# Kernel optimization log

Hardware: AMD Instinct MI355X
Metric: run time of the kernel (lower is better)

Reference implementation:

```python
import jax, jax.numpy as jnp
import numpy as np

EPS = 1e-5

def bn_lastdim(x, g, b):
    # BatchNorm2d (training-mode batch stats) applied over all axes except last channel axis
    m = x.mean(axis=(0, 1, 2), keepdims=True)
    v = x.var(axis=(0, 1, 2), keepdims=True)
    return g * (x - m) * jax.lax.rsqrt(v + EPS) + b

def setup_inputs() -> dict:
    key = jax.random.key(0)
    ks = jax.random.split(key, 8)
    B, N, M, F1, K = 8, 8192, 2048, 64, 32
    PF, OUT, DIV = 64, 128, 4
    IN_CH = PF + F1  # 128
    inp = {
        "points": jax.random.normal(ks[0], (B, N, 3), jnp.float32),
        "queries": jax.random.normal(ks[1], (B, M, 3), jnp.float32),
        "feat_prev": jax.random.normal(ks[2], (B, N, F1), jnp.float32),
        # Lift params: linear1 3->32, linear2 32->64
        "w1": jax.random.normal(ks[3], (3, PF // 2), jnp.float32) * 0.1,
        "b1": jnp.zeros((PF // 2,), jnp.float32),
        "w2": jax.random.normal(ks[4], (PF // 2, PF), jnp.float32) * 0.1,
        "b2": jnp.zeros((PF,), jnp.float32),
        # batchnorm affine params (bn1 over 3, bn2 over 32, bn3 over in_channel)
        "g1": jnp.ones((3,), jnp.float32), "be1": jnp.zeros((3,), jnp.float32),
        "g2": jnp.ones((PF // 2,), jnp.float32), "be2": jnp.zeros((PF // 2,), jnp.float32),
        "g3": jnp.ones((IN_CH,), jnp.float32), "be3": jnp.zeros((IN_CH,), jnp.float32),
        # conv2d (out, in, 1, division) -> drop singleton H dim
        "wc": jax.random.normal(ks[5], (OUT, IN_CH, DIV), jnp.float32) * 0.05,
        "bc": jnp.zeros((OUT,), jnp.float32),
    }
    return inp

def reference(points, queries, feat_prev, w1, b1, w2, b2, g1, be1, g2, be2, g3, be3, wc, bc):
    K = 32
    DIV = 4
    S = K // DIV  # maxpool window/stride along neighbor axis
    B = points.shape[0]

    # ---- KNN: squared distances (same ordering as torch.cdist + topk smallest) ----
    pn = jnp.sum(points * points, axis=-1)   # (B,N)
    qn = jnp.sum(queries * queries, axis=-1) # (B,M)
    d2 = qn[:, :, None] + pn[:, None, :] - 2.0 * jnp.einsum('bmd,bnd->bmn', queries, points)
    _, idx = jax.lax.top_k(-d2, K)           # idx: (B,M,K), sorted nearest-first

    batch_ix = jnp.arange(B)[:, None, None]
    knn_pts = points[batch_ix, idx]          # (B,M,K,3)
    local = queries[:, :, None, :] - knn_pts # (B,M,K,3)

    # ---- Lift MLP (with batchnorm, training-mode stats) ----
    h = bn_lastdim(local, g1, be1)
    h = jax.nn.relu(h @ w1 + b1)             # (B,M,K,32)
    h = bn_lastdim(h, g2, be2)
    h = jax.nn.relu(h @ w2 + b2)             # (B,M,K,64)

    # ---- gather previous features, concat ----
    knn_prev = feat_prev[batch_ix, idx]      # (B,M,K,F1)
    feat = jnp.concatenate([h, knn_prev], axis=-1)  # (B,M,K,C) C=128

    # ---- maxpool over neighbor axis (window S, stride S) ----
    Bq, M, _, C = feat.shape
    feat = feat.reshape(Bq, M, DIV, S, C).max(axis=3)  # (B,M,DIV,C)

    # ---- BN + conv2d kernel (1,DIV) + relu; width collapses to 1 ----
    feat = bn_lastdim(feat, g3, be3)
    out = jnp.einsum('bmdc,ocd->bmo', feat, wc) + bc
    return jax.nn.relu(out)                  # (B,M,out_features)
```

## Files before the change

### kernel.cpp

```cpp
#include <hip/hip_runtime.h>
#include <math.h>

#define B_   8
#define N_   8192
#define M_   2048
#define KNN  32
#define F1_  64
#define HID  32
#define DIV_ 4

typedef unsigned long long u64;
typedef unsigned int u32;

__global__ __launch_bounds__(256) void pack_kernel(
    const float* __restrict__ points, float4* __restrict__ ppk)
{
  const int i = blockIdx.x*256 + threadIdx.x;
  const float* pp = &points[(size_t)i*3];
  float px = pp[0], py = pp[1], pz = pp[2];
  float pn = __builtin_fmaf(pz, pz, __builtin_fmaf(py, py, __fmul_rn(px, px)));
  ppk[i] = make_float4(px, py, pz, pn);
}

__device__ __forceinline__ u32 ord_f32(float f) {
  u32 u = __float_as_uint(f);
  return u ^ (u32)(((int)u >> 31) | 0x80000000);
}

__global__ __launch_bounds__(256) void knn_kernel(
    const float4* __restrict__ ppk, const float* __restrict__ queries,
    int* __restrict__ idx_out, float* __restrict__ local_out)
{
  const int bid = blockIdx.x;
  const int b = bid >> 8;
  const int qbase = (bid & 255) * 8;
  const int t = threadIdx.x, lane = t & 63, wid = t >> 6;

  const int q0 = qbase + wid*2;
  float qx[2], qy[2], qz[2], qn[2];
  u64 c0[2], c1[2], c2[2];
  #pragma unroll
  for (int q = 0; q < 2; ++q) {
    int m = q0 + q;
    qx[q] = queries[(b*M_+m)*3+0];
    qy[q] = queries[(b*M_+m)*3+1];
    qz[q] = queries[(b*M_+m)*3+2];
    qn[q] = __builtin_fmaf(qz[q], qz[q], __builtin_fmaf(qy[q], qy[q], __fmul_rn(qx[q], qx[q])));
    c0[q] = c1[q] = c2[q] = ~0ull;
  }

  const float4* __restrict__ base = ppk + (size_t)b * N_;

  float4 pa = base[lane];
  float4 pb = base[64 + lane];
  #pragma unroll 4
  for (int j = 0; j < 128; ++j) {
    const float4 pc = (j + 2 < 128) ? base[(j+2)*64 + lane] : pa;
    const int n = j*64 + lane;
    #pragma unroll
    for (int q = 0; q < 2; ++q) {
      float dot = __builtin_fmaf(qz[q], pa.z, __builtin_fmaf(qy[q], pa.y, __fmul_rn(qx[q], pa.x)));
      float s   = __fadd_rn(qn[q], pa.w);
      float d2  = __builtin_fmaf(-2.0f, dot, s);
      u64 key = ((u64)ord_f32(d2) << 32) | (u32)n;
      u64 a0 = key < c0[q] ? key   : c0[q];
      u64 A0 = key < c0[q] ? c0[q] : key;
      u64 a1 = A0 < c1[q] ? A0    : c1[q];
      u64 A1 = A0 < c1[q] ? c1[q] : A0;
      u64 a2 = A1 < c2[q] ? A1    : c2[q];
      c0[q] = a0; c1[q] = a1; c2[q] = a2;
    }
    pa = pb; pb = pc;
  }

  u64 e0[2] = {c0[0], c0[1]}, e1[2] = {c1[0], c1[1]}, e2[2] = {c2[0], c2[1]};
  u64 cand[2] = {e0[0], e0[1]};
  u64 mykey[2] = {~0ull, ~0ull};
  int rem[2] = {3, 3};

  for (int r = 0; r < KNN; ++r) {
    u64 wa = cand[0], wb = cand[1];
    #pragma unroll
    for (int dlt = 1; dlt < 64; dlt <<= 1) {
      u64 oa = __shfl_xor(wa, dlt);
      u64 ob = __shfl_xor(wb, dlt);
      wa = oa < wa ? oa : wa;
      wb = ob < wb ? ob : wb;
    }
    if (lane == r) { mykey[0] = wa; mykey[1] = wb; }
    u64 w2q[2] = {wa, wb};
    #pragma unroll
    for (int q = 0; q < 2; ++q) {
      const u64 w = w2q[q];
      if (cand[q] == w) {
        e0[q] = e1[q]; e1[q] = e2[q]; e2[q] = ~0ull; --rem[q];
        if (rem[q] == 0) {
          const u64 lim = w;
          u64 f0 = ~0ull, f1 = ~0ull, f2 = ~0ull;
          for (int j = 0; j < 128; ++j) {
            int n = j*64 + lane;
            const float4 p = base[n];
            float dot = __builtin_fmaf(qz[q], p.z, __builtin_fmaf(qy[q], p.y, __fmul_rn(qx[q], p.x)));
            float d2  = __builtin_fmaf(-2.0f, dot, __fadd_rn(qn[q], p.w));
            u64 key = ((u64)ord_f32(d2) << 32) | (u32)n;
            if (key > lim) {
              u64 a0 = key < f0 ? key : f0;
              u64 A0 = key < f0 ? f0  : key;
              u64 a1 = A0 < f1 ? A0   : f1;
              u64 A1 = A0 < f1 ? f1   : A0;
              u64 a2 = A1 < f2 ? A1   : f2;
              f0 = a0; f1 = a1; f2 = a2;
            }
          }
          e0[q] = f0; e1[q] = f1; e2[q] = f2;
          rem[q] = (f2 != ~0ull) ? 3 : ((f1 != ~0ull) ? 2 : ((f0 != ~0ull) ? 1 : 0));
        }
        cand[q] = e0[q];
      }
    }
  }

  #pragma unroll
  for (int q = 0; q < 2; ++q) {
    if (lane < KNN) {
      u32 n = (u32)mykey[q];
      int bm = b*M_ + q0 + q;
      idx_out[bm*KNN + lane] = (int)n;
      const float4 p = base[n];
      local_out[(bm*KNN + lane)*3 + 0] = qx[q] - p.x;
      local_out[(bm*KNN + lane)*3 + 1] = qy[q] - p.y;
      local_out[(bm*KNN + lane)*3 + 2] = qz[q] - p.z;
    }
  }
}

__global__ __launch_bounds__(256) void bn1_stats_kernel(
    const float* __restrict__ local, float* __restrict__ p1)
{
  const int t = threadIdx.x;
  const int gid = blockIdx.x*256 + t;
  float s0=0,s1=0,s2=0,q0=0,q1=0,q2=0;
  for (int r = gid; r < B_*M_*KNN; r += 65536) {
    float a = local[r*3+0], b = local[r*3+1], c = local[r*3+2];
    s0 += a; s1 += b; s2 += c;
    q0 = fmaf(a,a,q0); q1 = fmaf(b,b,q1); q2 = fmaf(c,c,q2);
  }
  __shared__ float red[256][8];
  red[t][0]=s0; red[t][1]=s1; red[t][2]=s2; red[t][3]=0.f;
  red[t][4]=q0; red[t][5]=q1; red[t][6]=q2; red[t][7]=0.f;
  __syncthreads();
  for (int st = 128; st >= 1; st >>= 1) {
    if (t < st) {
      #pragma unroll
      for (int j = 0; j < 8; ++j) red[t][j] += red[t+st][j];
    }
    __syncthreads();
  }
  if (t < 8) p1[blockIdx.x*8 + t] = red[0][t];
}

__global__ __launch_bounds__(128) void bn1_fold_kernel(
    const float* __restrict__ p1, const float* __restrict__ g1, const float* __restrict__ be1,
    const float* __restrict__ w1, const float* __restrict__ b1, float* __restrict__ prm)
{
  __shared__ float sc[3], sh[3];
  const int t = threadIdx.x;
  if (t < 3) {
    double s = 0, q = 0;
    for (int blk = 0; blk < 256; ++blk) { s += p1[blk*8+t]; q += p1[blk*8+4+t]; }
    double n = (double)(B_*M_*KNN);
    double m = s/n, v = q/n - m*m;
    double rs = 1.0/sqrt(v + 1e-5);
    float scale = (float)((double)g1[t]*rs);
    sc[t] = scale; sh[t] = be1[t] - (float)m*scale;
  }
  __syncthreads();
  if (t < 96) prm[t] = w1[t]*sc[t/32];
  if (t < 32) {
    float a = b1[t];
    for (int c = 0; c < 3; ++c) a = fmaf(sh[c], w1[c*32+t], a);
    prm[96+t] = a;
  }
}

__global__ __launch_bounds__(256) void h1_stats_kernel(
    const float* __restrict__ local, const float* __restrict__ prm, float* __restrict__ p2)
{
  const int t = threadIdx.x;
  const int k4 = (t & 7) * 4;
  float w0[4], w1q[4], w2q[4], b1q[4];
  #pragma unroll
  for (int i = 0; i < 4; ++i) {
    w0[i]  = prm[ 0 + k4 + i];
    w1q[i] = prm[32 + k4 + i];
    w2q[i] = prm[64 + k4 + i];
    b1q[i] = prm[96 + k4 + i];
  }
  float s[4] = {0,0,0,0}, sq[4] = {0,0,0,0};
  const int r0 = (blockIdx.x*256 + t) >> 3;
  for (int r = r0; r < B_*M_*KNN; r += 16384) {
    float l0 = local[r*3+0], l1 = local[r*3+1], l2 = local[r*3+2];
    #pragma unroll
    for (int i = 0; i < 4; ++i) {
      float v = fmaf(l2, w2q[i], fmaf(l1, w1q[i], fmaf(l0, w0[i], b1q[i])));
      v = fmaxf(v, 0.0f);
      s[i] += v; sq[i] = fmaf(v, v, sq[i]);
    }
  }
  __shared__ float red[256][8];
  #pragma unroll
  for (int i = 0; i < 4; ++i) { red[t][i] = s[i]; red[t][4+i] = sq[i]; }
  __syncthreads();
  for (int st = 128; st >= 8; st >>= 1) {
    if (t < st) {
      #pragma unroll
      for (int j = 0; j < 8; ++j) red[t][j] += red[t+st][j];
    }
    __syncthreads();
  }
  if (t < 8) {
    #pragma unroll
    for (int i = 0; i < 4; ++i) {
      p2[blockIdx.x*64 +      t*4 + i] = red[t][i];
      p2[blockIdx.x*64 + 32 + t*4 + i] = red[t][4+i];
    }
  }
}

__global__ __launch_bounds__(64) void bn2_fold_kernel(
    const float* __restrict__ p2, const float* __restrict__ g2, const float* __restrict__ be2,
    const float* __restrict__ w2, const float* __restrict__ b2, float* __restrict__ prm)
{
  __shared__ float sc[32], sh[32];
  const int t = threadIdx.x;
  if (t < 32) {
    double s = 0, q = 0;
    for (int blk = 0; blk < 512; ++blk) { s += p2[blk*64+t]; q += p2[blk*64+32+t]; }
    double n = (double)(B_*M_*KNN);
    double m = s/n, v = q/n - m*m;
    double rs = 1.0/sqrt(v + 1e-5);
    float scale = (float)((double)g2[t]*rs);
    sc[t] = scale; sh[t] = be2[t] - (float)m*scale;
  }
  __syncthreads();
  {
    int j = t;
    float a = b2[j];
    for (int k = 0; k < 32; ++k) {
      float wv = w2[k*64 + j];
      prm[128 + j*32 + k] = wv * sc[k];
      a = fmaf(sh[k], wv, a);
    }
    prm[2176 + j] = a;
  }
}

__global__ __launch_bounds__(256) void h2_prev_pool_kernel(
    const float* __restrict__ local, const float* __restrict__ prm,
    const float* __restrict__ feat_prev, const int* __restrict__ idx,
    float* __restrict__ pooled)
{
  const int t = threadIdx.x;
  const int row = blockIdx.x*256 + t;
  const int bm = row >> 5, s = row & 31, d = s >> 3;
  const float l0 = local[row*3+0], l1 = local[row*3+1], l2 = local[row*3+2];
  float h1v[32];
  #pragma unroll
  for (int k = 0; k < 32; ++k) {
    float v = fmaf(l2, prm[64+k], fmaf(l1, prm[32+k], fmaf(l0, prm[0+k], prm[96+k])));
    h1v[k] = fmaxf(v, 0.0f);
  }
  const float* __restrict__ w2t = prm + 128;
  const float* __restrict__ b2f = prm + 2176;
  #pragma unroll 4
  for (int j = 0; j < 64; ++j) {
    float acc = b2f[j];
    #pragma unroll
    for (int k = 0; k < 32; ++k) acc = fmaf(h1v[k], w2t[j*32+k], acc);
    acc = fmaxf(acc, 0.0f);
    acc = fmaxf(acc, __shfl_xor(acc, 1));
    acc = fmaxf(acc, __shfl_xor(acc, 2));
    acc = fmaxf(acc, __shfl_xor(acc, 4));
    if ((s & 7) == 0) pooled[(bm*4 + d)*128 + j] = acc;
  }

  const int bm0 = blockIdx.x * 8;
  #pragma unroll
  for (int it = 0; it < 8; ++it) {
    const int task = it*256 + t;
    const int bmL  = task >> 8;
    const int dd   = (task >> 6) & 3;
    const int ch   = task & 63;
    const int bmg  = bm0 + bmL;
    const int bb   = bmg >> 11;
    float pm = -3.402823466e+38f;
    #pragma unroll
    for (int s8 = 0; s8 < 8; ++s8) {
      int n = idx[bmg*KNN + dd*8 + s8];
      float v = feat_prev[((size_t)(bb*N_ + n))*64 + ch];
      pm = fmaxf(pm, v);
    }
    pooled[(size_t)(bmg*4 + dd)*128 + 64 + ch] = pm;
  }
}

__global__ __launch_bounds__(256) void bn3_stats_kernel(
    const float* __restrict__ pooled, float* __restrict__ p3)
{
  const int t = threadIdx.x, c = t & 127, rr = t >> 7;
  float s = 0, q = 0;
  for (int r = blockIdx.x*2 + rr; r < B_*M_*DIV_; r += 512) {
    float v = pooled[(size_t)r*128 + c];
    s += v; q = fmaf(v, v, q);
  }
  __shared__ float red[256][2];
  red[t][0] = s; red[t][1] = q;
  __syncthreads();
  if (t < 128) {
    p3[blockIdx.x*256 +       t] = red[t][0] + red[t+128][0];
    p3[blockIdx.x*256 + 128 + t] = red[t][1] + red[t+128][1];
  }
}

__global__ __launch_bounds__(256) void bn3_fold_kernel(
    const float* __restrict__ p3, const float* __restrict__ g3, const float* __restrict__ be3,
    const float* __restrict__ wc, const float* __restrict__ bc, float* __restrict__ prm)
{
  __shared__ float sc[128], sh[128];
  const int t = threadIdx.x;
  if (t < 128) {
    double s = 0, q = 0;
    for (int blk = 0; blk < 256; ++blk) { s += p3[blk*256+t]; q += p3[blk*256+128+t]; }
    double n = (double)(B_*M_*DIV_);
    double m = s/n, v = q/n - m*m;
    double rs = 1.0/sqrt(v + 1e-5);
    float scale = (float)((double)g3[t]*rs);
    sc[t] = scale; sh[t] = be3[t] - (float)m*scale;
  }
  __syncthreads();
  for (int e = t; e < 512*128; e += 256) {
    int i = e >> 7, o = e & 127, dd = i >> 7, cc = i & 127;
    prm[2240 + e] = wc[o*512 + cc*4 + dd] * sc[cc];
  }
  if (t < 128) {
    int o = t;
    float a = bc[o];
    for (int cc = 0; cc < 128; ++cc) {
      float hsum = 0;
      #pragma unroll
      for (int dd = 0; dd < 4; ++dd) hsum += wc[o*512 + cc*4 + dd];
      a = fmaf(sh[cc], hsum, a);
    }
    prm[67776 + o] = a;
  }
}

__global__ __launch_bounds__(256) void conv_gemm_kernel(
    const float* __restrict__ pooled, const float* __restrict__ prm,
    float* __restrict__ outp)
{
  const float* __restrict__ Bw  = prm + 2240;
  const float* __restrict__ bcf = prm + 67776;
  __shared__ float As[32][68];
  __shared__ float Bs[32][128];
  const int t = threadIdx.x;
  const int cg = t & 15, rg = t >> 4;
  const int rowbase = blockIdx.x * 64;
  float acc[4][8];
  #pragma unroll
  for (int i = 0; i < 4; ++i)
    #pragma unroll
    for (int j = 0; j < 8; ++j) acc[i][j] = 0.f;

  float bb[8];
  #pragma unroll
  for (int j = 0; j < 8; ++j) bb[j] = bcf[cg*8 + j];

  for (int k0 = 0; k0 < 512; k0 += 32) {
    #pragma unroll
    for (int li = t; li < 512; li += 256) {
      int r = li >> 3, qd = li & 7;
      const float4 v = *(const float4*)&pooled[(size_t)(rowbase+r)*512 + k0 + qd*4];
      As[qd*4+0][r] = v.x; As[qd*4+1][r] = v.y; As[qd*4+2][r] = v.z; As[qd*4+3][r] = v.w;
    }
    #pragma unroll
    for (int i = 0; i < 4; ++i) {
      int li = t + i*256;
      int kk = li >> 5, c4 = (li & 31) * 4;
      *(float4*)&Bs[kk][c4] = *(const float4*)&Bw[(size_t)(k0+kk)*128 + c4];
    }
    __syncthreads();
    #pragma unroll 8
    for (int kk = 0; kk < 32; ++kk) {
      float4 a  = *(const float4*)&As[kk][rg*4];
      float4 b0 = *(const float4*)&Bs[kk][cg*8];
      float4 b1 = *(const float4*)&Bs[kk][cg*8+4];
      float av[4] = {a.x, a.y, a.z, a.w};
      float bv[8] = {b0.x, b0.y, b0.z, b0.w, b1.x, b1.y, b1.z, b1.w};
      #pragma unroll
      for (int i = 0; i < 4; ++i)
        #pragma unroll
        for (int j = 0; j < 8; ++j)
          acc[i][j] = fmaf(av[i], bv[j], acc[i][j]);
    }
    __syncthreads();
  }
  #pragma unroll
  for (int i = 0; i < 4; ++i) {
    int r = rowbase + rg*4 + i;
    float4 o0, o1;
    o0.x = fmaxf(acc[i][0] + bb[0], 0.f);
    o0.y = fmaxf(acc[i][1] + bb[1], 0.f);
    o0.z = fmaxf(acc[i][2] + bb[2], 0.f);
    o0.w = fmaxf(acc[i][3] + bb[3], 0.f);
    o1.x = fmaxf(acc[i][4] + bb[4], 0.f);
    o1.y = fmaxf(acc[i][5] + bb[5], 0.f);
    o1.z = fmaxf(acc[i][6] + bb[6], 0.f);
    o1.w = fmaxf(acc[i][7] + bb[7], 0.f);
    *(float4*)&outp[(size_t)r*128 + cg*8    ] = o0;
    *(float4*)&outp[(size_t)r*128 + cg*8 + 4] = o1;
  }
}

extern "C" void kernel_launch(void* const* d_in, const int* in_sizes, int n_in,
                              void* d_out, int out_size, void* d_ws, size_t ws_size,
                              hipStream_t stream)
{
  (void)in_sizes; (void)n_in; (void)out_size; (void)ws_size;
  const float* points    = (const float*)d_in[0];
  const float* queries   = (const float*)d_in[1];
  const float* feat_prev = (const float*)d_in[2];
  const float* w1  = (const float*)d_in[3];
  const float* b1  = (const float*)d_in[4];
  const float* w2  = (const float*)d_in[5];
  const float* b2  = (const float*)d_in[6];
  const float* g1  = (const float*)d_in[7];
  const float* be1 = (const float*)d_in[8];
  const float* g2  = (const float*)d_in[9];
  const float* be2 = (const float*)d_in[10];
  const float* g3  = (const float*)d_in[11];
  const float* be3 = (const float*)d_in[12];
  const float* wc  = (const float*)d_in[13];
  const float* bc  = (const float*)d_in[14];
  float* outp = (float*)d_out;

  char* ws = (char*)d_ws;
  int*   idx    = (int*)ws;
  float* local  = (float*)(ws + (2u<<20));
  float* pooled = (float*)(ws + (8u<<20));
  float* prm    = (float*)(ws + (40u<<20));
  float* p1     = (float*)(ws + (41u<<20));
  float* p2     = p1 + 4096;
  float* p3     = p2 + 32768;
  float4* ppk   = (float4*)(ws + (42u<<20));

  pack_kernel    <<<256,   256, 0, stream>>>(points, ppk);
  knn_kernel     <<<2048,  256, 0, stream>>>(ppk, queries, idx, local);
  bn1_stats_kernel<<<256,  256, 0, stream>>>(local, p1);
  bn1_fold_kernel<<<1,     128, 0, stream>>>(p1, g1, be1, w1, b1, prm);
  h1_stats_kernel<<<512,   256, 0, stream>>>(local, prm, p2);
  bn2_fold_kernel<<<1,      64, 0, stream>>>(p2, g2, be2, w2, b2, prm);
  h2_prev_pool_kernel<<<2048, 256, 0, stream>>>(local, prm, feat_prev, idx, pooled);
  bn3_stats_kernel<<<256,  256, 0, stream>>>(pooled, p3);
  bn3_fold_kernel<<<1,     256, 0, stream>>>(p3, g3, be3, wc, bc, prm);
  conv_gemm_kernel<<<256,  256, 0, stream>>>(pooled, prm, outp);
}
```

Measured before the change: 613.4 us.

## Fuse BN stats, folds and pooling into one cooperative grid-synced kernel

Replaces seven small launches (three BN stat reductions, three single-block fold kernels, and the lift/pool kernel) with one cooperative kernel of 512 blocks that separates the phases with grid.sync. The intent is to remove launch gaps and the serial tail of the 1-block fold kernels. The KNN loop is also restructured: the edge-case branch on the prefetch is peeled out, the unroll is lowered and occupancy is hinted with launch_bounds. In exchange, grid-wide barriers cost some latency, the fused lift phase gets less parallelism per block, and the old path remains only as a fallback if the cooperative launch fails.

```diff
diff --git a/kernel.cpp b/kernel.cpp
--- a/kernel.cpp
+++ b/kernel.cpp
@@ -1,5 +1,8 @@
 #include <hip/hip_runtime.h>
+#include <hip/hip_cooperative_groups.h>
 #include <math.h>
+
+namespace cg = cooperative_groups;
 
 #define B_   8
 #define N_   8192
@@ -8,6 +11,7 @@
 #define F1_  64
 #define HID  32
 #define DIV_ 4
+#define NB_  512
 
 typedef unsigned long long u64;
 typedef unsigned int u32;
@@ -27,7 +31,26 @@
   return u ^ (u32)(((int)u >> 31) | 0x80000000);
 }
 
-__global__ __launch_bounds__(256) void knn_kernel(
+#define KNN_INSERT(PV, NV)                                                    \
+  {                                                                           \
+    const int n_ = (NV);                                                      \
+    _Pragma("unroll")                                                         \
+    for (int q = 0; q < 2; ++q) {                                             \
+      float dot = __builtin_fmaf(qz[q], (PV).z,                               \
+                  __builtin_fmaf(qy[q], (PV).y, __fmul_rn(qx[q], (PV).x)));   \
+      float s_  = __fadd_rn(qn[q], (PV).w);                                   \
+      float d2  = __builtin_fmaf(-2.0f, dot, s_);                             \
+      u64 key = ((u64)ord_f32(d2) << 32) | (u32)n_;                           \
+      u64 a0 = key < c0[q] ? key   : c0[q];                                   \
+      u64 A0 = key < c0[q] ? c0[q] : key;                                     \
+      u64 a1 = A0 < c1[q] ? A0    : c1[q];                                    \
+      u64 A1 = A0 < c1[q] ? c1[q] : A0;                                      \
+      u64 a2 = A1 < c2[q] ? A1    : c2[q];                                   \
+      c0[q] = a0; c1[q] = a1; c2[q] = a2;                                    \
+    }                                                                         \
+  }
+
+__global__ __launch_bounds__(256, 6) void knn_kernel(
     const float4* __restrict__ ppk, const float* __restrict__ queries,
     int* __restrict__ idx_out, float* __restrict__ local_out)
 {
@@ -53,25 +76,14 @@
 
   float4 pa = base[lane];
   float4 pb = base[64 + lane];
-  #pragma unroll 4
-  for (int j = 0; j < 128; ++j) {
-    const float4 pc = (j + 2 < 128) ? base[(j+2)*64 + lane] : pa;
-    const int n = j*64 + lane;
-    #pragma unroll
-    for (int q = 0; q < 2; ++q) {
-      float dot = __builtin_fmaf(qz[q], pa.z, __builtin_fmaf(qy[q], pa.y, __fmul_rn(qx[q], pa.x)));
-      float s   = __fadd_rn(qn[q], pa.w);
-      float d2  = __builtin_fmaf(-2.0f, dot, s);
-      u64 key = ((u64)ord_f32(d2) << 32) | (u32)n;
-      u64 a0 = key < c0[q] ? key   : c0[q];
-      u64 A0 = key < c0[q] ? c0[q] : key;
-      u64 a1 = A0 < c1[q] ? A0    : c1[q];
-      u64 A1 = A0 < c1[q] ? c1[q] : A0;
-      u64 a2 = A1 < c2[q] ? A1    : c2[q];
-      c0[q] = a0; c1[q] = a1; c2[q] = a2;
-    }
+  #pragma unroll 2
+  for (int j = 0; j < 126; ++j) {
+    const float4 pc = base[(j+2)*64 + lane];
+    KNN_INSERT(pa, j*64 + lane);
     pa = pb; pb = pc;
   }
+  KNN_INSERT(pa, 126*64 + lane);
+  KNN_INSERT(pb, 127*64 + lane);
 
   u64 e0[2] = {c0[0], c0[1]}, e1[2] = {c1[0], c1[1]}, e2[2] = {c2[0], c2[1]};
   u64 cand[2] = {e0[0], e0[1]};
@@ -134,6 +146,233 @@
   }
 }
 
+__global__ __launch_bounds__(256, 4) void mid_coop_kernel(
+    const float* __restrict__ local,
+    const float* __restrict__ g1, const float* __restrict__ be1,
+    const float* __restrict__ w1, const float* __restrict__ b1,
+    const float* __restrict__ g2, const float* __restrict__ be2,
+    const float* __restrict__ w2, const float* __restrict__ b2,
+    const float* __restrict__ g3, const float* __restrict__ be3,
+    const float* __restrict__ wc, const float* __restrict__ bc,
+    const float* __restrict__ feat_prev, const int* __restrict__ idx,
+    float* __restrict__ pooled, float* __restrict__ prm,
+    float* __restrict__ p1, float* __restrict__ p2, float* __restrict__ p3)
+{
+  cg::grid_group grid = cg::this_grid();
+  const int t = threadIdx.x, bid = blockIdx.x;
+  __shared__ float red[256][8];
+
+  {
+    float s0=0,s1=0,s2=0,q0=0,q1=0,q2=0;
+    for (int r = bid*256 + t; r < B_*M_*KNN; r += NB_*256) {
+      float a = local[r*3+0], b = local[r*3+1], c = local[r*3+2];
+      s0 += a; s1 += b; s2 += c;
+      q0 = fmaf(a,a,q0); q1 = fmaf(b,b,q1); q2 = fmaf(c,c,q2);
+    }
+    red[t][0]=s0; red[t][1]=s1; red[t][2]=s2; red[t][3]=0.f;
+    red[t][4]=q0; red[t][5]=q1; red[t][6]=q2; red[t][7]=0.f;
+    __syncthreads();
+    for (int st = 128; st >= 1; st >>= 1) {
+      if (t < st) {
+        #pragma unroll
+        for (int j = 0; j < 8; ++j) red[t][j] += red[t+st][j];
+      }
+      __syncthreads();
+    }
+    if (t < 8) p1[bid*8 + t] = red[0][t];
+  }
+  __threadfence();
+  grid.sync();
+
+  if (bid == 0) {
+    if (t < 3) {
+      double s = 0, q = 0;
+      for (int blk = 0; blk < NB_; ++blk) { s += p1[blk*8+t]; q += p1[blk*8+4+t]; }
+      double n = (double)(B_*M_*KNN);
+      double m = s/n, v = q/n - m*m;
+      double rs = 1.0/sqrt(v + 1e-5);
+      float scale = (float)((double)g1[t]*rs);
+      red[0][t] = scale;
+      red[1][t] = be1[t] - (float)m*scale;
+    }
+    __syncthreads();
+    if (t < 96) prm[t] = w1[t]*red[0][t/32];
+    if (t < 32) {
+      float a = b1[t];
+      for (int c = 0; c < 3; ++c) a = fmaf(red[1][c], w1[c*32+t], a);
+      prm[96+t] = a;
+    }
+  }
+  __threadfence();
+  grid.sync();
+
+  {
+    const int k4 = (t & 7) * 4;
+    float w0[4], w1q[4], w2q[4], b1q[4];
+    #pragma unroll
+    for (int i = 0; i < 4; ++i) {
+      w0[i]  = prm[ 0 + k4 + i];
+      w1q[i] = prm[32 + k4 + i];
+      w2q[i] = prm[64 + k4 + i];
+      b1q[i] = prm[96 + k4 + i];
+    }
+    float s[4] = {0,0,0,0}, sq[4] = {0,0,0,0};
+    const int r0 = (bid*256 + t) >> 3;
+    for (int r = r0; r < B_*M_*KNN; r += (NB_*256) >> 3) {
+      float l0 = local[r*3+0], l1 = local[r*3+1], l2 = local[r*3+2];
+      #pragma unroll
+      for (int i = 0; i < 4; ++i) {
+        float v = fmaf(l2, w2q[i], fmaf(l1, w1q[i], fmaf(l0, w0[i], b1q[i])));
+        v = fmaxf(v, 0.0f);
+        s[i] += v; sq[i] = fmaf(v, v, sq[i]);
+      }
+    }
+    __syncthreads();
+    #pragma unroll
+    for (int i = 0; i < 4; ++i) { red[t][i] = s[i]; red[t][4+i] = sq[i]; }
+    __syncthreads();
+    for (int st = 128; st >= 8; st >>= 1) {
+      if (t < st) {
+        #pragma unroll
+        for (int j = 0; j < 8; ++j) red[t][j] += red[t+st][j];
+      }
+      __syncthreads();
+    }
+    if (t < 8) {
+      #pragma unroll
+      for (int i = 0; i < 4; ++i) {
+        p2[bid*64 +      t*4 + i] = red[t][i];
+        p2[bid*64 + 32 + t*4 + i] = red[t][4+i];
+      }
+    }
+  }
+  __threadfence();
+  grid.sync();
+
+  if (bid == 0) {
+    if (t < 32) {
+      double s = 0, q = 0;
+      for (int blk = 0; blk < NB_; ++blk) { s += p2[blk*64+t]; q += p2[blk*64+32+t]; }
+      double n = (double)(B_*M_*KNN);
+      double m = s/n, v = q/n - m*m;
+      double rs = 1.0/sqrt(v + 1e-5);
+      float scale = (float)((double)g2[t]*rs);
+      red[t][0] = scale;
+      red[t][1] = be2[t] - (float)m*scale;
+    }
+    __syncthreads();
+    if (t < 64) {
+      int j = t;
+      float a = b2[j];
+      for (int k = 0; k < 32; ++k) {
+        float wv = w2[k*64 + j];
+        prm[128 + j*32 + k] = wv * red[k][0];
+        a = fmaf(red[k][1], wv, a);
+      }
+      prm[2176 + j] = a;
+    }
+  }
+  __threadfence();
+  grid.sync();
+
+  {
+    const float* __restrict__ w2t = prm + 128;
+    const float* __restrict__ b2f = prm + 2176;
+    for (int it = 0; it < (B_*M_*KNN)/(NB_*256); ++it) {
+      const int row = it*NB_*256 + bid*256 + t;
+      const int bm = row >> 5, s = row & 31, d = s >> 3;
+      const float l0 = local[row*3+0], l1 = local[row*3+1], l2 = local[row*3+2];
+      float h1v[32];
+      #pragma unroll
+      for (int k = 0; k < 32; ++k) {
+        float v = fmaf(l2, prm[64+k], fmaf(l1, prm[32+k], fmaf(l0, prm[0+k], prm[96+k])));
+        h1v[k] = fmaxf(v, 0.0f);
+      }
+      #pragma unroll 4
+      for (int j = 0; j < 64; ++j) {
+        float acc = b2f[j];
+        #pragma unroll
+        for (int k = 0; k < 32; ++k) acc = fmaf(h1v[k], w2t[j*32+k], acc);
+        acc = fmaxf(acc, 0.0f);
+        acc = fmaxf(acc, __shfl_xor(acc, 1));
+        acc = fmaxf(acc, __shfl_xor(acc, 2));
+        acc = fmaxf(acc, __shfl_xor(acc, 4));
+        if ((s & 7) == 0) pooled[(bm*4 + d)*128 + j] = acc;
+      }
+    }
+    for (int it = 0; it < (B_*M_*DIV_*64)/(NB_*256); ++it) {
+      const int task = it*NB_*256 + bid*256 + t;
+      const int bmg = task >> 8;
+      const int dd  = (task >> 6) & 3;
+      const int ch  = task & 63;
+      const int bb  = bmg >> 11;
+      float pm = -3.402823466e+38f;
+      #pragma unroll
+      for (int s8 = 0; s8 < 8; ++s8) {
+        int n = idx[bmg*KNN + dd*8 + s8];
+        float v = feat_prev[((size_t)(bb*N_ + n))*64 + ch];
+        pm = fmaxf(pm, v);
+      }
+      pooled[(size_t)(bmg*4 + dd)*128 + 64 + ch] = pm;
+    }
+  }
+  __threadfence();
+  grid.sync();
+
+  {
+    const int c = t & 127, rr = t >> 7;
+    float s = 0, q = 0;
+    for (int r = bid*2 + rr; r < B_*M_*DIV_; r += NB_*2) {
+      float v = pooled[(size_t)r*128 + c];
+      s += v; q = fmaf(v, v, q);
+    }
+    __syncthreads();
+    red[t][0] = s; red[t][1] = q;
+    __syncthreads();
+    if (t < 128) {
+      p3[bid*256 +       t] = red[t][0] + red[t+128][0];
+      p3[bid*256 + 128 + t] = red[t][1] + red[t+128][1];
+    }
+  }
+  __threadfence();
+  grid.sync();
+
+  if (bid == 0) {
+    if (t < 128) {
+      double s = 0, q = 0;
+      for (int blk = 0; blk < NB_; ++blk) { s += p3[blk*256+t]; q += p3[blk*256+128+t]; }
+      double n = (double)(B_*M_*DIV_);
+      double m = s/n, v = q/n - m*m;
+      double rs = 1.0/sqrt(v + 1e-5);
+      float scale = (float)((double)g3[t]*rs);
+      prm[68096 + t] = scale;
+      prm[68224 + t] = be3[t] - (float)m*scale;
+    }
+    __syncthreads();
+    if (t < 128) {
+      int o = t;
+      float a = bc[o];
+      for (int cc = 0; cc < 128; ++cc) {
+        float hsum = 0;
+        #pragma unroll
+        for (int dd = 0; dd < 4; ++dd) hsum += wc[o*512 + cc*4 + dd];
+        a = fmaf(prm[68224 + cc], hsum, a);
+      }
+      prm[67776 + o] = a;
+    }
+  }
+  __threadfence();
+  grid.sync();
+
+  {
+    const int e = bid*256 + t;
+    if (e < 512*128) {
+      int i = e >> 7, o = e & 127, dd = i >> 7, cc = i & 127;
+      prm[2240 + e] = wc[o*512 + cc*4 + dd] * prm[68096 + cc];
+    }
+  }
+}
+
 __global__ __launch_bounds__(256) void bn1_stats_kernel(
     const float* __restrict__ local, float* __restrict__ p1)
 {
@@ -283,7 +522,6 @@
     acc = fmaxf(acc, __shfl_xor(acc, 4));
     if ((s & 7) == 0) pooled[(bm*4 + d)*128 + j] = acc;
   }
-
   const int bm0 = blockIdx.x * 8;
   #pragma unroll
   for (int it = 0; it < 8; ++it) {
@@ -364,7 +602,7 @@
   __shared__ float As[32][68];
   __shared__ float Bs[32][128];
   const int t = threadIdx.x;
-  const int cg = t & 15, rg = t >> 4;
+  const int cg_ = t & 15, rg = t >> 4;
   const int rowbase = blockIdx.x * 64;
   float acc[4][8];
   #pragma unroll
@@ -374,7 +612,7 @@
 
   float bb[8];
   #pragma unroll
-  for (int j = 0; j < 8; ++j) bb[j] = bcf[cg*8 + j];
+  for (int j = 0; j < 8; ++j) bb[j] = bcf[cg_*8 + j];
 
   for (int k0 = 0; k0 < 512; k0 += 32) {
     #pragma unroll
@@ -393,8 +631,8 @@
     #pragma unroll 8
     for (int kk = 0; kk < 32; ++kk) {
       float4 a  = *(const float4*)&As[kk][rg*4];
-      float4 b0 = *(const float4*)&Bs[kk][cg*8];
-      float4 b1 = *(const float4*)&Bs[kk][cg*8+4];
+      float4 b0 = *(const float4*)&Bs[kk][cg_*8];
+      float4 b1 = *(const float4*)&Bs[kk][cg_*8+4];
       float av[4] = {a.x, a.y, a.z, a.w};
       float bv[8] = {b0.x, b0.y, b0.z, b0.w, b1.x, b1.y, b1.z, b1.w};
       #pragma unroll
@@ -417,8 +655,8 @@
     o1.y = fmaxf(acc[i][5] + bb[5], 0.f);
     o1.z = fmaxf(acc[i][6] + bb[6], 0.f);
     o1.w = fmaxf(acc[i][7] + bb[7], 0.f);
-    *(float4*)&outp[(size_t)r*128 + cg*8    ] = o0;
-    *(float4*)&outp[(size_t)r*128 + cg*8 + 4] = o1;
+    *(float4*)&outp[(size_t)r*128 + cg_*8    ] = o0;
+    *(float4*)&outp[(size_t)r*128 + cg_*8 + 4] = o1;
   }
 }
 
@@ -450,18 +688,31 @@
   float* pooled = (float*)(ws + (8u<<20));
   float* prm    = (float*)(ws + (40u<<20));
   float* p1     = (float*)(ws + (41u<<20));
-  float* p2     = p1 + 4096;
-  float* p3     = p2 + 32768;
+  float* p2     = p1 + 8192;
   float4* ppk   = (float4*)(ws + (42u<<20));
+  float* p3     = (float*)(ws + (43u<<20));
 
   pack_kernel    <<<256,   256, 0, stream>>>(points, ppk);
   knn_kernel     <<<2048,  256, 0, stream>>>(ppk, queries, idx, local);
-  bn1_stats_kernel<<<256,  256, 0, stream>>>(local, p1);
-  bn1_fold_kernel<<<1,     128, 0, stream>>>(p1, g1, be1, w1, b1, prm);
-  h1_stats_kernel<<<512,   256, 0, stream>>>(local, prm, p2);
-  bn2_fold_kernel<<<1,      64, 0, stream>>>(p2, g2, be2, w2, b2, prm);
-  h2_prev_pool_kernel<<<2048, 256, 0, stream>>>(local, prm, feat_prev, idx, pooled);
-  bn3_stats_kernel<<<256,  256, 0, stream>>>(pooled, p3);
-  bn3_fold_kernel<<<1,     256, 0, stream>>>(p3, g3, be3, wc, bc, prm);
+
+  void* cargs[] = {
+    (void*)&local, (void*)&g1, (void*)&be1, (void*)&w1, (void*)&b1,
+    (void*)&g2, (void*)&be2, (void*)&w2, (void*)&b2,
+    (void*)&g3, (void*)&be3, (void*)&wc, (void*)&bc,
+    (void*)&feat_prev, (void*)&idx,
+    (void*)&pooled, (void*)&prm, (void*)&p1, (void*)&p2, (void*)&p3
+  };
+  hipError_t cerr = hipLaunchCooperativeKernel((const void*)mid_coop_kernel,
+                                               dim3(NB_), dim3(256), cargs, 0, stream);
+  if (cerr != hipSuccess) {
+    bn1_stats_kernel<<<256,  256, 0, stream>>>(local, p1);
+    bn1_fold_kernel<<<1,     128, 0, stream>>>(p1, g1, be1, w1, b1, prm);
+    h1_stats_kernel<<<512,   256, 0, stream>>>(local, prm, p2);
+    bn2_fold_kernel<<<1,      64, 0, stream>>>(p2, g2, be2, w2, b2, prm);
+    h2_prev_pool_kernel<<<2048, 256, 0, stream>>>(local, prm, feat_prev, idx, pooled);
+    bn3_stats_kernel<<<256,  256, 0, stream>>>(pooled, p3);
+    bn3_fold_kernel<<<1,     256, 0, stream>>>(p3, g3, be3, wc, bc, prm);
+  }
+
   conv_gemm_kernel<<<256,  256, 0, stream>>>(pooled, prm, outp);
 }
```

Result: slower. 1.261 ms (+105.6%).
